# Kernel optimization log

Measured on AMD Instinct MI355X. Metric: run time of the kernel, lower is better.

## Reference

```python
import jax, jax.numpy as jnp
import numpy as np

BLOCK = 32  # GGML Q8_0-style block size: one scale per 32 quantized values


def setup_inputs() -> dict:
    key = jax.random.key(0)
    k1, k2, k3, k4 = jax.random.split(key, 4)
    B, S, IN, OUT = 2, 4096, 4096, 4096
    inp = jax.random.normal(k1, (B, S, IN), dtype=jnp.float32)
    # stored GGUF layout: [in_features, out_features]; torch forward transposes it
    qweight = jax.random.randint(k2, (IN, OUT), -127, 128, dtype=jnp.int32)  # int8 codes
    scales = jax.random.normal(k3, (IN, OUT // BLOCK), dtype=jnp.float32) * 0.01  # per-block scale
    bias = jax.random.normal(k4, (OUT,), dtype=jnp.float32) * 0.02
    return {"input": inp, "qweight": qweight, "scales": scales, "bias": bias}


def _dequantize(qweight, scales, dtype):
    # blockwise dequant: w[i, b*32 + j] = q[i, b*32 + j] * scale[i, b]
    IN, OUT = qweight.shape
    q = qweight.reshape(IN, OUT // BLOCK, BLOCK).astype(dtype)
    return (q * scales[:, :, None].astype(dtype)).reshape(IN, OUT)


def reference(input, qweight, scales, bias):
    # torch: F.linear(x, W_stored.T, b) == x @ W_stored + b with W_stored [IN, OUT]
    w = _dequantize(qweight, scales, input.dtype)  # [IN, OUT]
    return jnp.einsum('bsi,io->bso', input, w) + bias
```

## Files before the change

### kernel.cpp

```cpp
#include <hip/hip_runtime.h>
#include <hip/hip_bf16.h>
#include <stdint.h>


#define M_DIM 8192
#define N_DIM 4096
#define K_DIM 4096
#define NBLK  128

typedef __attribute__((ext_vector_type(8))) short short8;
typedef __attribute__((ext_vector_type(4))) float f32x4;

typedef const __attribute__((address_space(1))) unsigned char* gas;
typedef __attribute__((address_space(3))) unsigned char* las;

__device__ __forceinline__ unsigned pk_bf16(float a, float b) {
  unsigned ua = __builtin_bit_cast(unsigned, a);
  unsigned ub = __builtin_bit_cast(unsigned, b);
  ua += 0x7fffu + ((ua >> 16) & 1u);
  ub += 0x7fffu + ((ub >> 16) & 1u);
  return (ua >> 16) | (ub & 0xffff0000u);
}

__global__ __launch_bounds__(256)
void a_to_bf16(const float* __restrict__ A, ushort* __restrict__ Abf) {
  const long idx = ((long)blockIdx.x * 256 + threadIdx.x) * 8;
  const float4 v0 = *(const float4*)(A + idx);
  const float4 v1 = *(const float4*)(A + idx + 4);
  uint4 p;
  p.x = pk_bf16(v0.x, v0.y);
  p.y = pk_bf16(v0.z, v0.w);
  p.z = pk_bf16(v1.x, v1.y);
  p.w = pk_bf16(v1.z, v1.w);
  *(uint4*)(Abf + idx) = p;
}

__global__ __launch_bounds__(256)
void dequant_transpose(const int* __restrict__ Q, const float* __restrict__ S,
                       ushort* __restrict__ Wt) {
  __shared__ ushort T[64 * 68];
  const int k0 = blockIdx.y * 64;
  const int n0 = blockIdx.x * 64;
  const int t = threadIdx.x;
  const int nl = t & 63;
  const int kb = t >> 6;

  const float sscale = S[0] * 0.0f;
  (void)sscale;

  #pragma unroll
  for (int i = 0; i < 16; ++i) {
    const int kl = kb + i * 4;
    const int k = k0 + kl;
    const int q = Q[(long)k * N_DIM + n0 + nl];
    const float s = S[k * NBLK + ((n0 + nl) >> 5)];
    const float w = (float)q * s;
    unsigned u = __builtin_bit_cast(unsigned, w);
    u += 0x7fffu + ((u >> 16) & 1u);
    T[nl * 68 + kl] = (ushort)(u >> 16);
  }
  __syncthreads();

  const int n = t >> 2;
  const int kc = (t & 3) * 16;
  const ushort* src = &T[n * 68 + kc];
  uint2 a = *(const uint2*)(src + 0);
  uint2 b = *(const uint2*)(src + 4);
  uint2 c = *(const uint2*)(src + 8);
  uint2 d = *(const uint2*)(src + 12);
  uint4 o0 = {a.x, a.y, b.x, b.y};
  uint4 o1 = {c.x, c.y, d.x, d.y};
  ushort* dst = Wt + (long)(n0 + n) * K_DIM + k0 + kc;
  *(uint4*)(dst + 0) = o0;
  *(uint4*)(dst + 8) = o1;
}

__global__ __launch_bounds__(256)
void gemm_bf16(const ushort* __restrict__ Abf, const ushort* __restrict__ Wt,
               const float* __restrict__ bias, float* __restrict__ C) {
  __shared__ __align__(16) ushort Alds[128 * 32];
  __shared__ __align__(16) ushort Blds[128 * 32];

  const int tid = threadIdx.x;
  const int m0 = blockIdx.y * 128;
  const int n0 = blockIdx.x * 128;
  const int wave = tid >> 6;
  const int lane = tid & 63;
  const int wm = (wave >> 1) * 64;
  const int wn = (wave & 1) * 64;
  const int lrow = lane & 15;
  const int quad = lane >> 4;

  const int srow = wave * 16 + (lane >> 2);
  const int skoff = (lane & 3) * 8;

  const ushort* Ag0 = Abf + (long)(m0 + srow) * K_DIM + skoff;
  const ushort* Ag1 = Ag0 + (long)64 * K_DIM;
  const ushort* Bg0 = Wt + (long)(n0 + srow) * K_DIM + skoff;
  const ushort* Bg1 = Bg0 + (long)64 * K_DIM;

  ushort* Al0 = &Alds[wave * 512];
  ushort* Al1 = &Alds[wave * 512 + 2048];
  ushort* Bl0 = &Blds[wave * 512];
  ushort* Bl1 = &Blds[wave * 512 + 2048];

  f32x4 acc[4][4];
  #pragma unroll
  for (int i = 0; i < 4; ++i)
    #pragma unroll
    for (int j = 0; j < 4; ++j)
      acc[i][j] = (f32x4){0.f, 0.f, 0.f, 0.f};

  for (int k0 = 0; k0 < K_DIM; k0 += 32) {
    __builtin_amdgcn_global_load_lds((gas)(Ag0 + k0), (las)Al0, 16, 0, 0);
    __builtin_amdgcn_global_load_lds((gas)(Ag1 + k0), (las)Al1, 16, 0, 0);
    __builtin_amdgcn_global_load_lds((gas)(Bg0 + k0), (las)Bl0, 16, 0, 0);
    __builtin_amdgcn_global_load_lds((gas)(Bg1 + k0), (las)Bl1, 16, 0, 0);
    __syncthreads();

    short8 afrag[4], bfrag[4];
    #pragma unroll
    for (int t = 0; t < 4; ++t) {
      afrag[t] = *(const short8*)&Alds[(wm + t * 16 + lrow) * 32 + quad * 8];
      bfrag[t] = *(const short8*)&Blds[(wn + t * 16 + lrow) * 32 + quad * 8];
    }
    #pragma unroll
    for (int mt = 0; mt < 4; ++mt)
      #pragma unroll
      for (int nt = 0; nt < 4; ++nt)
        acc[mt][nt] = __builtin_amdgcn_mfma_f32_16x16x32_bf16(afrag[mt], bfrag[nt],
                                                              acc[mt][nt], 0, 0, 0);
    __syncthreads();
  }

  #pragma unroll
  for (int nt = 0; nt < 4; ++nt) {
    const int n = n0 + wn + nt * 16 + lrow;
    const float bv = bias[n];
    #pragma unroll
    for (int mt = 0; mt < 4; ++mt) {
      const int mbase = m0 + wm + mt * 16 + quad * 4;
      #pragma unroll
      for (int r = 0; r < 4; ++r) {
        C[(long)(mbase + r) * N_DIM + n] = acc[mt][nt][r] + bv;
      }
    }
  }
}

__global__ __launch_bounds__(256)
void gguf_gemm_fused(const float* __restrict__ A, const int* __restrict__ Q,
                     const float* __restrict__ S, const float* __restrict__ bias,
                     float* __restrict__ C) {
  __shared__ __align__(16) ushort Alds[128 * 32];
  __shared__ __align__(16) ushort Blds[128 * 32];
  const int tid = threadIdx.x;
  const int m0 = blockIdx.y * 128;
  const int n0 = blockIdx.x * 128;
  const int wave = tid >> 6, lane = tid & 63;
  const int wm = (wave >> 1) * 64, wn = (wave & 1) * 64;
  const int lrow = lane & 15, quad = lane >> 4;
  const int ar = tid >> 2, ac = (tid & 3) * 4;
  const int c8a = ((ar >> 1) & 3) << 3;
  const int bn = tid & 127, bkc = (tid >> 7) * 16;
  const int c8b = ((bn >> 1) & 3) << 3;
  const float* Abase = A + (long)(m0 + ar) * K_DIM + ac;
  const int* Qbase = Q + (long)bkc * N_DIM + n0 + bn;
  const float* Sbase = S + (long)bkc * NBLK + ((n0 + bn) >> 5);
  f32x4 acc[4][4];
  #pragma unroll
  for (int i = 0; i < 4; ++i)
    #pragma unroll
    for (int j = 0; j < 4; ++j) acc[i][j] = (f32x4){0.f, 0.f, 0.f, 0.f};
  for (int k0 = 0; k0 < K_DIM; k0 += 32) {
    #pragma unroll
    for (int i = 0; i < 2; ++i)
      #pragma unroll
      for (int j = 0; j < 2; ++j) {
        const float4 v = *(const float4*)(Abase + (long)i * 64 * K_DIM + k0 + j * 16);
        uint2 p; p.x = pk_bf16(v.x, v.y); p.y = pk_bf16(v.z, v.w);
        const int k = ac + j * 16;
        *(uint2*)&Alds[(ar + i * 64) * 32 + (k ^ c8a)] = p;
      }
    {
      const int* qp = Qbase + (long)k0 * N_DIM;
      const float* sp = Sbase + (long)k0 * NBLK;
      unsigned w[8];
      #pragma unroll
      for (int i = 0; i < 8; ++i) {
        const int q0 = qp[(2 * i) * N_DIM];
        const int q1 = qp[(2 * i + 1) * N_DIM];
        const float s0 = sp[(2 * i) * NBLK];
        const float s1 = sp[(2 * i + 1) * NBLK];
        w[i] = pk_bf16((float)q0 * s0, (float)q1 * s1);
      }
      uint4 g0 = {w[0], w[1], w[2], w[3]};
      uint4 g1 = {w[4], w[5], w[6], w[7]};
      *(uint4*)&Blds[bn * 32 + (bkc ^ c8b)] = g0;
      *(uint4*)&Blds[bn * 32 + ((bkc + 8) ^ c8b)] = g1;
    }
    __syncthreads();
    short8 afrag[4], bfrag[4];
    #pragma unroll
    for (int t = 0; t < 4; ++t) {
      const int mrow = wm + t * 16 + lrow;
      afrag[t] = *(const short8*)&Alds[mrow * 32 + ((quad * 8) ^ (((mrow >> 1) & 3) << 3))];
      const int nrow = wn + t * 16 + lrow;
      bfrag[t] = *(const short8*)&Blds[nrow * 32 + ((quad * 8) ^ (((nrow >> 1) & 3) << 3))];
    }
    #pragma unroll
    for (int mt = 0; mt < 4; ++mt)
      #pragma unroll
      for (int nt = 0; nt < 4; ++nt)
        acc[mt][nt] = __builtin_amdgcn_mfma_f32_16x16x32_bf16(afrag[mt], bfrag[nt],
                                                              acc[mt][nt], 0, 0, 0);
    __syncthreads();
  }
  #pragma unroll
  for (int nt = 0; nt < 4; ++nt) {
    const int n = n0 + wn + nt * 16 + lrow;
    const float bv = bias[n];
    #pragma unroll
    for (int mt = 0; mt < 4; ++mt) {
      const int mbase = m0 + wm + mt * 16 + quad * 4;
      #pragma unroll
      for (int r = 0; r < 4; ++r)
        C[(long)(mbase + r) * N_DIM + n] = acc[mt][nt][r] + bv;
    }
  }
}

extern "C" void kernel_launch(void* const* d_in, const int* in_sizes, int n_in,
                              void* d_out, int out_size, void* d_ws, size_t ws_size,
                              hipStream_t stream) {
  const float* A    = (const float*)d_in[0];
  const int*   Q    = (const int*)d_in[1];
  const float* S    = (const float*)d_in[2];
  const float* bias = (const float*)d_in[3];
  float* C = (float*)d_out;

  const size_t abf_bytes = (size_t)M_DIM * K_DIM * 2;
  const size_t wt_bytes  = (size_t)N_DIM * K_DIM * 2;

  if (ws_size >= abf_bytes + wt_bytes) {
    ushort* Abf = (ushort*)d_ws;
    ushort* Wt  = (ushort*)((char*)d_ws + abf_bytes);
    a_to_bf16<<<(M_DIM * (long)K_DIM) / (256 * 8), 256, 0, stream>>>(A, Abf);
    dim3 gt(N_DIM / 64, K_DIM / 64);
    dequant_transpose<<<gt, 256, 0, stream>>>(Q, S, Wt);
    dim3 grid(N_DIM / 128, M_DIM / 128);
    gemm_bf16<<<grid, 256, 0, stream>>>(Abf, Wt, bias, C);
  } else {
    dim3 grid(N_DIM / 128, M_DIM / 128);
    gguf_gemm_fused<<<grid, 256, 0, stream>>>(A, Q, S, bias, C);
  }
}
```

Baseline: 574.3 us.

## Merge prep kernels and double GEMM K-tile with XOR-swizzled LDS

The activation-to-bf16 conversion and the weight dequant-transpose are merged into one launch, with block ranges selecting the job. This removes a kernel launch and lets both prep jobs run concurrently. The GEMM main loop now stages 64-wide K tiles instead of 32, which halves the number of barriers per K. It also XOR-swizzles the LDS chunk placement to avoid bank conflicts on the fragment reads. LDS use doubles, which may reduce occupancy, and the loop still has no double buffering.

```diff
diff --git a/kernel.cpp b/kernel.cpp
--- a/kernel.cpp
+++ b/kernel.cpp
@@ -23,63 +23,59 @@
 }
 
 __global__ __launch_bounds__(256)
-void a_to_bf16(const float* __restrict__ A, ushort* __restrict__ Abf) {
-  const long idx = ((long)blockIdx.x * 256 + threadIdx.x) * 8;
-  const float4 v0 = *(const float4*)(A + idx);
-  const float4 v1 = *(const float4*)(A + idx + 4);
-  uint4 p;
-  p.x = pk_bf16(v0.x, v0.y);
-  p.y = pk_bf16(v0.z, v0.w);
-  p.z = pk_bf16(v1.x, v1.y);
-  p.w = pk_bf16(v1.z, v1.w);
-  *(uint4*)(Abf + idx) = p;
-}
-
-__global__ __launch_bounds__(256)
-void dequant_transpose(const int* __restrict__ Q, const float* __restrict__ S,
-                       ushort* __restrict__ Wt) {
+void prep(const float* __restrict__ A, const int* __restrict__ Q,
+          const float* __restrict__ S, ushort* __restrict__ Abf,
+          ushort* __restrict__ Wt) {
   __shared__ ushort T[64 * 68];
-  const int k0 = blockIdx.y * 64;
-  const int n0 = blockIdx.x * 64;
   const int t = threadIdx.x;
-  const int nl = t & 63;
-  const int kb = t >> 6;
-
-  const float sscale = S[0] * 0.0f;
-  (void)sscale;
-
-  #pragma unroll
-  for (int i = 0; i < 16; ++i) {
-    const int kl = kb + i * 4;
-    const int k = k0 + kl;
-    const int q = Q[(long)k * N_DIM + n0 + nl];
-    const float s = S[k * NBLK + ((n0 + nl) >> 5)];
-    const float w = (float)q * s;
-    unsigned u = __builtin_bit_cast(unsigned, w);
-    u += 0x7fffu + ((u >> 16) & 1u);
-    T[nl * 68 + kl] = (ushort)(u >> 16);
-  }
-  __syncthreads();
-
-  const int n = t >> 2;
-  const int kc = (t & 3) * 16;
-  const ushort* src = &T[n * 68 + kc];
-  uint2 a = *(const uint2*)(src + 0);
-  uint2 b = *(const uint2*)(src + 4);
-  uint2 c = *(const uint2*)(src + 8);
-  uint2 d = *(const uint2*)(src + 12);
-  uint4 o0 = {a.x, a.y, b.x, b.y};
-  uint4 o1 = {c.x, c.y, d.x, d.y};
-  ushort* dst = Wt + (long)(n0 + n) * K_DIM + k0 + kc;
-  *(uint4*)(dst + 0) = o0;
-  *(uint4*)(dst + 8) = o1;
+  if (blockIdx.x < 16384) {
+    const long idx = ((long)blockIdx.x * 256 + t) * 8;
+    const float4 v0 = *(const float4*)(A + idx);
+    const float4 v1 = *(const float4*)(A + idx + 4);
+    uint4 p;
+    p.x = pk_bf16(v0.x, v0.y);
+    p.y = pk_bf16(v0.z, v0.w);
+    p.z = pk_bf16(v1.x, v1.y);
+    p.w = pk_bf16(v1.z, v1.w);
+    *(uint4*)(Abf + idx) = p;
+  } else {
+    const int bid = blockIdx.x - 16384;
+    const int n0 = (bid & 63) * 64;
+    const int k0 = (bid >> 6) * 64;
+    const int nl = t & 63;
+    const int kb = t >> 6;
+    #pragma unroll
+    for (int i = 0; i < 16; ++i) {
+      const int kl = kb + i * 4;
+      const int k = k0 + kl;
+      const int q = Q[(long)k * N_DIM + n0 + nl];
+      const float s = S[k * NBLK + ((n0 + nl) >> 5)];
+      const float w = (float)q * s;
+      unsigned u = __builtin_bit_cast(unsigned, w);
+      u += 0x7fffu + ((u >> 16) & 1u);
+      T[nl * 68 + kl] = (ushort)(u >> 16);
+    }
+    __syncthreads();
+    const int n = t >> 2;
+    const int kc = (t & 3) * 16;
+    const ushort* src = &T[n * 68 + kc];
+    uint2 a = *(const uint2*)(src + 0);
+    uint2 b = *(const uint2*)(src + 4);
+    uint2 c = *(const uint2*)(src + 8);
+    uint2 d = *(const uint2*)(src + 12);
+    uint4 o0 = {a.x, a.y, b.x, b.y};
+    uint4 o1 = {c.x, c.y, d.x, d.y};
+    ushort* dst = Wt + (long)(n0 + n) * K_DIM + k0 + kc;
+    *(uint4*)(dst + 0) = o0;
+    *(uint4*)(dst + 8) = o1;
+  }
 }
 
 __global__ __launch_bounds__(256)
 void gemm_bf16(const ushort* __restrict__ Abf, const ushort* __restrict__ Wt,
                const float* __restrict__ bias, float* __restrict__ C) {
-  __shared__ __align__(16) ushort Alds[128 * 32];
-  __shared__ __align__(16) ushort Blds[128 * 32];
+  __shared__ __align__(16) ushort Alds[128 * 64];
+  __shared__ __align__(16) ushort Blds[128 * 64];
 
   const int tid = threadIdx.x;
   const int m0 = blockIdx.y * 128;
@@ -91,18 +87,11 @@
   const int lrow = lane & 15;
   const int quad = lane >> 4;
 
-  const int srow = wave * 16 + (lane >> 2);
-  const int skoff = (lane & 3) * 8;
-
-  const ushort* Ag0 = Abf + (long)(m0 + srow) * K_DIM + skoff;
-  const ushort* Ag1 = Ag0 + (long)64 * K_DIM;
-  const ushort* Bg0 = Wt + (long)(n0 + srow) * K_DIM + skoff;
-  const ushort* Bg1 = Bg0 + (long)64 * K_DIM;
-
-  ushort* Al0 = &Alds[wave * 512];
-  ushort* Al1 = &Alds[wave * 512 + 2048];
-  ushort* Bl0 = &Blds[wave * 512];
-  ushort* Bl1 = &Blds[wave * 512 + 2048];
+  const int srow = wave * 8 + (lane >> 3);
+  const int schunk = (lane & 7) ^ ((lane >> 3) & 7);
+
+  const ushort* Ag = Abf + (long)(m0 + srow) * K_DIM + schunk * 8;
+  const ushort* Bg = Wt + (long)(n0 + srow) * K_DIM + schunk * 8;
 
   f32x4 acc[4][4];
   #pragma unroll
@@ -111,25 +100,34 @@
     for (int j = 0; j < 4; ++j)
       acc[i][j] = (f32x4){0.f, 0.f, 0.f, 0.f};
 
-  for (int k0 = 0; k0 < K_DIM; k0 += 32) {
-    __builtin_amdgcn_global_load_lds((gas)(Ag0 + k0), (las)Al0, 16, 0, 0);
-    __builtin_amdgcn_global_load_lds((gas)(Ag1 + k0), (las)Al1, 16, 0, 0);
-    __builtin_amdgcn_global_load_lds((gas)(Bg0 + k0), (las)Bl0, 16, 0, 0);
-    __builtin_amdgcn_global_load_lds((gas)(Bg1 + k0), (las)Bl1, 16, 0, 0);
-    __syncthreads();
-
-    short8 afrag[4], bfrag[4];
-    #pragma unroll
-    for (int t = 0; t < 4; ++t) {
-      afrag[t] = *(const short8*)&Alds[(wm + t * 16 + lrow) * 32 + quad * 8];
-      bfrag[t] = *(const short8*)&Blds[(wn + t * 16 + lrow) * 32 + quad * 8];
-    }
-    #pragma unroll
-    for (int mt = 0; mt < 4; ++mt)
-      #pragma unroll
-      for (int nt = 0; nt < 4; ++nt)
-        acc[mt][nt] = __builtin_amdgcn_mfma_f32_16x16x32_bf16(afrag[mt], bfrag[nt],
-                                                              acc[mt][nt], 0, 0, 0);
+  const int pswz = (quad ^ (lane & 7)) * 8;
+
+  for (int k0 = 0; k0 < K_DIM; k0 += 64) {
+    #pragma unroll
+    for (int i = 0; i < 4; ++i) {
+      __builtin_amdgcn_global_load_lds((gas)(Ag + (long)i * 32 * K_DIM + k0),
+                                       (las)&Alds[(wave * 8 + i * 32) * 64], 16, 0, 0);
+      __builtin_amdgcn_global_load_lds((gas)(Bg + (long)i * 32 * K_DIM + k0),
+                                       (las)&Blds[(wave * 8 + i * 32) * 64], 16, 0, 0);
+    }
+    __syncthreads();
+
+    #pragma unroll
+    for (int h = 0; h < 2; ++h) {
+      const int pb = pswz ^ (h << 5);
+      short8 af[4], bf[4];
+      #pragma unroll
+      for (int t = 0; t < 4; ++t) {
+        af[t] = *(const short8*)&Alds[(wm + t * 16 + lrow) * 64 + pb];
+        bf[t] = *(const short8*)&Blds[(wn + t * 16 + lrow) * 64 + pb];
+      }
+      #pragma unroll
+      for (int mt = 0; mt < 4; ++mt)
+        #pragma unroll
+        for (int nt = 0; nt < 4; ++nt)
+          acc[mt][nt] = __builtin_amdgcn_mfma_f32_16x16x32_bf16(af[mt], bf[nt],
+                                                                acc[mt][nt], 0, 0, 0);
+    }
     __syncthreads();
   }
 
@@ -245,9 +243,7 @@
   if (ws_size >= abf_bytes + wt_bytes) {
     ushort* Abf = (ushort*)d_ws;
     ushort* Wt  = (ushort*)((char*)d_ws + abf_bytes);
-    a_to_bf16<<<(M_DIM * (long)K_DIM) / (256 * 8), 256, 0, stream>>>(A, Abf);
-    dim3 gt(N_DIM / 64, K_DIM / 64);
-    dequant_transpose<<<gt, 256, 0, stream>>>(Q, S, Wt);
+    prep<<<16384 + 4096, 256, 0, stream>>>(A, Q, S, Abf, Wt);
     dim3 grid(N_DIM / 128, M_DIM / 128);
     gemm_bf16<<<grid, 256, 0, stream>>>(Abf, Wt, bias, C);
   } else {
```

Result: slower. 591.5 us (+3.0%).
